# Kernel optimization log

Measured on AMD Instinct MI355X. Metric: run time of the kernel, lower is better.

## Reference

```python
import jax, jax.numpy as jnp
import numpy as np

T = 2048        # num tokens
HID = 2048      # hidden_size
HQ = 16         # num_heads
HKV = 8         # num_kv_heads
D = 128         # head_dim
P = 2           # power retention exponent
THETA = 10000.0 # rope base
SCALE = D ** -0.5


def setup_inputs() -> dict:
    key = jax.random.key(0)
    ks = jax.random.split(key, 8)
    s = 0.02
    return {
        "positions": jnp.arange(T, dtype=jnp.int64) if jax.config.jax_enable_x64 else jnp.arange(T, dtype=jnp.int32),
        "hidden_states": jax.random.normal(ks[0], (T, HID), jnp.float32),
        "Wq": jax.random.normal(ks[1], (HID, HQ * D), jnp.float32) * s,
        "bq": jnp.zeros((HQ * D,), jnp.float32),
        "Wk": jax.random.normal(ks[2], (HID, HKV * D), jnp.float32) * s,
        "bk": jnp.zeros((HKV * D,), jnp.float32),
        "Wv": jax.random.normal(ks[3], (HID, HKV * D), jnp.float32) * s,
        "bv": jnp.zeros((HKV * D,), jnp.float32),
        "Wg": jax.random.normal(ks[4], (HID, HKV), jnp.float32) * s,
        "bg": jnp.zeros((HKV,), jnp.float32),
        "Wo": jax.random.normal(ks[5], (HQ * D, HID), jnp.float32) * s,
        "bo": jnp.zeros((HID,), jnp.float32),
    }


def _rope_neox(x, pos):
    # x: [T, H, D], pos: [T]; rotate-half (neox) style, rotary_dim == head_dim
    half = D // 2
    inv_freq = 1.0 / (THETA ** (jnp.arange(0, D, 2, dtype=jnp.float32) / D))  # [D/2]
    freqs = pos.astype(jnp.float32)[:, None] * inv_freq                        # [T, D/2]
    cos = jnp.cos(freqs)[:, None, :]
    sin = jnp.sin(freqs)[:, None, :]
    x1, x2 = x[..., :half], x[..., half:]
    return jnp.concatenate([x1 * cos - x2 * sin, x2 * cos + x1 * sin], axis=-1)


def reference(positions, hidden_states, Wq, bq, Wk, bk, Wv, bv, Wg, bg, Wo, bo):
    # QKVG projections
    q = (hidden_states @ Wq + bq).reshape(T, HQ, D)
    k = (hidden_states @ Wk + bk).reshape(T, HKV, D)
    v = (hidden_states @ Wv + bv).reshape(T, HKV, D)
    g = hidden_states @ Wg + bg            # [T, HKV], one gate scalar per kv head

    # RoPE on q/k, logsigmoid gate in fp32
    q = _rope_neox(q, positions)
    k = _rope_neox(k, positions)
    g = jax.nn.log_sigmoid(g.astype(jnp.float32))   # [T, HKV], <= 0
    G = jnp.cumsum(g, axis=0)                       # [T, HKV] cumulative log-decay

    # GQA: expand kv heads to query heads
    rep = HQ // HKV
    k = jnp.repeat(k, rep, axis=1)   # [T, HQ, D]
    v = jnp.repeat(v, rep, axis=1)
    G = jnp.repeat(G, rep, axis=1)   # [T, HQ]

    # Power retention (quadratic attention form, seq_len <= switch_over_seq_len):
    # W_ij = (scale * q_i . k_j)^p * exp(G_i - G_j), causal j <= i
    S = jnp.einsum('thd,shd->hts', q, k) * SCALE      # [H, T, T]
    S = S ** P
    Gh = G.T                                          # [H, T]
    mask = jnp.tril(jnp.ones((T, T), dtype=bool))
    diff = jnp.where(mask[None], Gh[:, :, None] - Gh[:, None, :], -jnp.inf)
    W = S * jnp.exp(diff)                             # decay<=1 inside mask, 0 outside

    out = jnp.einsum('hts,shd->thd', W, v)            # [T, H, D]
    out = out.reshape(T, HQ * D) @ Wo + bo            # o_proj
    return out
```

## Files before the change

### kernel.cpp

```cpp
#include <hip/hip_runtime.h>
#include <hip/hip_bf16.h>
#include <math.h>

#define T_SEQ 2048
#define HID 2048
#define HQ 16
#define HKV 8
#define D_HEAD 128
#define HALF 64
#define SCALE_F 0.08838834764831845f
#define PROJW 4096

typedef __attribute__((ext_vector_type(8))) short bf16x8;
typedef __attribute__((ext_vector_type(4))) float f32x4;

static __device__ __forceinline__ short f2bf(float x) {
  unsigned u = __builtin_bit_cast(unsigned, x);
  unsigned r = (u + 0x7FFF + ((u >> 16) & 1)) >> 16;
  return (short)r;
}
static __device__ __forceinline__ float bf2f(unsigned short u) {
  unsigned v = ((unsigned)u) << 16;
  return __builtin_bit_cast(float, v);
}

#define GLDS(gsrc, ldst) \
  __builtin_amdgcn_global_load_lds((const __attribute__((address_space(1))) void*)(gsrc), \
                                   (__attribute__((address_space(3))) void*)(ldst), 16, 0, 0)

__global__ __launch_bounds__(256)
void cvt_bf16(const float* __restrict__ in, short* __restrict__ out, int n4)
{
  int i = blockIdx.x * blockDim.x + threadIdx.x;
  if (i >= n4) return;
  float4 v = reinterpret_cast<const float4*>(in)[i];
  short4 o;
  o.x = f2bf(v.x); o.y = f2bf(v.y); o.z = f2bf(v.z); o.w = f2bf(v.w);
  reinterpret_cast<short4*>(out)[i] = o;
}

__global__ __launch_bounds__(256)
void transpose_to_bf16(const float* __restrict__ in, short* __restrict__ out,
                       int N, int out_ld)
{
  __shared__ float tile[32][33];
  const int k0 = blockIdx.y * 32, n0 = blockIdx.x * 32;
  const int r = threadIdx.x >> 5, c = threadIdx.x & 31;
  #pragma unroll
  for (int i = 0; i < 4; ++i)
    tile[r + i * 8][c] = in[(size_t)(k0 + r + i * 8) * N + n0 + c];
  __syncthreads();
  #pragma unroll
  for (int i = 0; i < 4; ++i)
    out[(size_t)(n0 + r + i * 8) * out_ld + k0 + c] = f2bf(tile[c][r + i * 8]);
}

__global__ __launch_bounds__(256)
void pack_bias(const float* __restrict__ bq, const float* __restrict__ bk,
               const float* __restrict__ bv, float* __restrict__ bcat)
{
  const int i = blockIdx.x * 256 + threadIdx.x;
  bcat[i] = (i < 2048) ? bq[i] : ((i < 3072) ? bk[i - 2048] : bv[i - 3072]);
}

__global__ __launch_bounds__(256)
void add_f32(float* __restrict__ out, const float* __restrict__ part, int n4)
{
  int i = blockIdx.x * blockDim.x + threadIdx.x;
  if (i >= n4) return;
  float4 a = reinterpret_cast<float4*>(out)[i];
  const float4 b = reinterpret_cast<const float4*>(part)[i];
  a.x += b.x; a.y += b.y; a.z += b.z; a.w += b.w;
  reinterpret_cast<float4*>(out)[i] = a;
}

template <bool OBF>
__global__ __launch_bounds__(256)
void gemm_bf16(const short* __restrict__ A, const short* __restrict__ BT,
               const float* __restrict__ bias, void* __restrict__ Cout0,
               void* __restrict__ Cout1, int N, int Kst, int klen)
{
  __shared__ short As[2][128 * 32];
  __shared__ short Bs[2][128 * 32];
  const int tid = threadIdx.x;
  const int wave = tid >> 6, lane = tid & 63;
  const int bm0 = blockIdx.y * 128, bn0 = blockIdx.x * 128;
  const int z = blockIdx.z;
  const int koff = z * klen;
  const int wm = (wave >> 1) * 64, wn = (wave & 1) * 64;

  const int srow = wave * 32 + (lane >> 2);
  const int scol = (lane & 3) * 8;
  const short* Abase = A + (size_t)(bm0 + srow) * Kst + koff + scol;
  const short* Bbase = BT + (size_t)(bn0 + srow) * Kst + koff + scol;

  f32x4 acc[4][4] = {};

  const int nk = klen >> 5;
#define STAGE(buf, k0)                                                        \
  do {                                                                        \
    GLDS(Abase + (k0), &As[buf][(wave * 32) * 32]);                           \
    GLDS(Abase + (k0) + (size_t)16 * Kst, &As[buf][(wave * 32 + 16) * 32]);   \
    GLDS(Bbase + (k0), &Bs[buf][(wave * 32) * 32]);                           \
    GLDS(Bbase + (k0) + (size_t)16 * Kst, &Bs[buf][(wave * 32 + 16) * 32]);   \
  } while (0)

  STAGE(0, 0);
  __syncthreads();

  const int kof = (lane >> 4) * 8;
  const int rA = wm + (lane & 15);
  const int rB = wn + (lane & 15);

  for (int t = 0; t < nk; ++t) {
    const int cur = t & 1;
    if (t + 1 < nk) STAGE(cur ^ 1, (t + 1) << 5);
    bf16x8 af[4], bfr[4];
    #pragma unroll
    for (int i = 0; i < 4; ++i) {
      af[i]  = *reinterpret_cast<const bf16x8*>(&As[cur][(rA + i * 16) * 32 + kof]);
      bfr[i] = *reinterpret_cast<const bf16x8*>(&Bs[cur][(rB + i * 16) * 32 + kof]);
    }
    #pragma unroll
    for (int i = 0; i < 4; ++i)
      #pragma unroll
      for (int j = 0; j < 4; ++j)
        acc[i][j] = __builtin_amdgcn_mfma_f32_16x16x32_bf16(af[i], bfr[j], acc[i][j], 0, 0, 0);
    __syncthreads();
  }

  void* Cout = z ? Cout1 : Cout0;
  const int crow = wm + (lane >> 4) * 4;
  const int ccol = wn + (lane & 15);
  #pragma unroll
  for (int j = 0; j < 4; ++j) {
    const int col = bn0 + ccol + j * 16;
    const float b = z ? 0.f : bias[col];
    #pragma unroll
    for (int i = 0; i < 4; ++i)
      #pragma unroll
      for (int r = 0; r < 4; ++r) {
        const int row = bm0 + crow + i * 16 + r;
        const float v = acc[i][j][r] + b;
        if constexpr (OBF)
          ((short*)Cout)[(size_t)row * N + col] = f2bf(v);
        else
          ((float*)Cout)[(size_t)row * N + col] = v;
      }
  }
#undef STAGE
}

__global__ __launch_bounds__(256)
void gproj_kernel(const float* __restrict__ hs, const float* __restrict__ Wg,
                  const float* __restrict__ bg, float* __restrict__ gT)
{
  const int t = blockIdx.x, tid = threadIdx.x;
  __shared__ float red[256][9];
  float a[8] = {0.f, 0.f, 0.f, 0.f, 0.f, 0.f, 0.f, 0.f};
  for (int cc = tid; cc < HID; cc += 256) {
    const float hv = hs[(size_t)t * HID + cc];
    const float4 w0 = *reinterpret_cast<const float4*>(Wg + (size_t)cc * 8);
    const float4 w1 = *reinterpret_cast<const float4*>(Wg + (size_t)cc * 8 + 4);
    a[0] = fmaf(hv, w0.x, a[0]); a[1] = fmaf(hv, w0.y, a[1]);
    a[2] = fmaf(hv, w0.z, a[2]); a[3] = fmaf(hv, w0.w, a[3]);
    a[4] = fmaf(hv, w1.x, a[4]); a[5] = fmaf(hv, w1.y, a[5]);
    a[6] = fmaf(hv, w1.z, a[6]); a[7] = fmaf(hv, w1.w, a[7]);
  }
  #pragma unroll
  for (int j = 0; j < 8; ++j) red[tid][j] = a[j];
  __syncthreads();
  for (int s = 128; s >= 1; s >>= 1) {
    if (tid < s) {
      #pragma unroll
      for (int j = 0; j < 8; ++j) red[tid][j] += red[tid + s][j];
    }
    __syncthreads();
  }
  if (tid < 8) {
    const float x = red[0][tid] + bg[tid];
    const float nx = -x;
    const float sp = (nx > 20.f) ? nx : log1pf(expf(nx));
    gT[(size_t)tid * T_SEQ + t] = -sp;
  }
}

__global__ __launch_bounds__(512)
void gscan_kernel(const float* __restrict__ gT, float* __restrict__ Gct)
{
  const int h = blockIdx.x;
  const int tid = threadIdx.x;
  const int wid = tid >> 6, lane = tid & 63;
  __shared__ float wsum[8];

  const float4 v = reinterpret_cast<const float4*>(gT + (size_t)h * T_SEQ)[tid];
  const float p0 = v.x, p1 = p0 + v.y, p2 = p1 + v.z, p3 = p2 + v.w;

  float sc = p3;
  #pragma unroll
  for (int off = 1; off < 64; off <<= 1) {
    const float o = __shfl_up(sc, off, 64);
    if (lane >= off) sc += o;
  }
  if (lane == 63) wsum[wid] = sc;
  __syncthreads();
  float wof = 0.f;
  #pragma unroll
  for (int w = 0; w < 8; ++w) wof += (w < wid) ? wsum[w] : 0.f;

  const float excl = wof + sc - p3;
  reinterpret_cast<float4*>(Gct + (size_t)h * T_SEQ)[tid] =
      make_float4(excl + p0, excl + p1, excl + p2, excl + p3);
}

__global__ __launch_bounds__(192)
void rope_kernel(short* __restrict__ proj)
{
  const int t = blockIdx.x;
  __shared__ float cs[64], sn[64];
  if (threadIdx.x < 64) {
    const int i = threadIdx.x;
    const float f = (float)t * powf(10000.0f, -(float)i / 64.0f);
    cs[i] = cosf(f); sn[i] = sinf(f);
  }
  __syncthreads();
  const int u = threadIdx.x;
  const int hh = u >> 3, ch = u & 7;
  short* base = proj + (size_t)t * PROJW +
                ((hh < HQ) ? hh * D_HEAD : 2048 + (hh - HQ) * D_HEAD);
  bf16x8 x1 = *reinterpret_cast<bf16x8*>(base + ch * 8);
  bf16x8 x2 = *reinterpret_cast<bf16x8*>(base + HALF + ch * 8);
  #pragma unroll
  for (int j = 0; j < 8; ++j) {
    const float a = bf2f((unsigned short)x1[j]);
    const float b = bf2f((unsigned short)x2[j]);
    const float cc = cs[ch * 8 + j], ss = sn[ch * 8 + j];
    x1[j] = f2bf(a * cc - b * ss);
    x2[j] = f2bf(b * cc + a * ss);
  }
  *reinterpret_cast<bf16x8*>(base + ch * 8) = x1;
  *reinterpret_cast<bf16x8*>(base + HALF + ch * 8) = x2;
}

__global__ __launch_bounds__(256)
void vtrans_kernel(const unsigned short* __restrict__ proj, unsigned short* __restrict__ vt)
{
  __shared__ unsigned short tile[32][33];
  const int tt = blockIdx.x * 32, dd = blockIdx.y * 32, hk = blockIdx.z;
  const int c = threadIdx.x & 31, r0 = (threadIdx.x >> 5) * 4;
  #pragma unroll
  for (int i = 0; i < 4; ++i)
    tile[r0 + i][c] = proj[(size_t)(tt + r0 + i) * PROJW + 3072 + hk * 128 + dd + c];
  __syncthreads();
  #pragma unroll
  for (int i = 0; i < 4; ++i)
    vt[(size_t)(hk * 128 + dd + r0 + i) * T_SEQ + tt + c] = tile[c][r0 + i];
}

__global__ __launch_bounds__(256, 1)
void attn_mfma(const short* __restrict__ proj, const short* __restrict__ vt,
               const float* __restrict__ Gct, short* __restrict__ outb)
{
  __shared__ __align__(16) char smem[86528];
  const int hk = blockIdx.x;
  const int tb = blockIdx.y * 64;
  const int tid = threadIdx.x;
  const int wid = tid >> 6, lane = tid & 63;
  const int c = lane & 15, g = lane >> 4;
  const int h = 2 * hk + (wid >> 1);
  const int tw = tb + (wid & 1) * 32;
  const float* Gh = Gct + (size_t)hk * T_SEQ;

  const float glim = Gh[tb] + 90.0f;
  int lo = 0, hi = tb;
  while (lo < hi) {
    const int mid = (lo + hi) >> 1;
    if (Gh[mid] > glim) lo = mid + 1; else hi = mid;
  }
  const int sfirst = lo & ~63;
  const int nst = ((tb - sfirst) >> 6) + 1;

  bf16x8 qf[2][4];
  #pragma unroll
  for (int tt = 0; tt < 2; ++tt)
    #pragma unroll
    for (int kb = 0; kb < 4; ++kb)
      qf[tt][kb] = *reinterpret_cast<const bf16x8*>(
          proj + (size_t)(tw + 16 * tt + c) * PROJW + h * D_HEAD + kb * 32 + g * 8);
  const float gt0 = Gh[tw + c];
  const float gt1 = Gh[tw + 16 + c];
  const float gtw = Gh[tw];
  const int twmax = tw + 31;

  f32x4 accv[2][8] = {};

#define ASTG(buf, s64)                                                                   \
  do {                                                                                   \
    _Pragma("unroll")                                                                    \
    for (int i2 = 0; i2 < 4; ++i2) {                                                     \
      const int cid = tid + 256 * i2;                                                    \
      const int kr = cid >> 4, kc = cid & 15;                                            \
      GLDS(proj + (size_t)((s64) + kr) * PROJW + 2048 + hk * 128 + ((kc ^ (kr & 7)) * 8),\
           smem + (buf) * 16384 + cid * 16);                                             \
      const int vr = cid >> 3, vc = cid & 7;                                             \
      GLDS(vt + (size_t)(hk * 128 + vr) * T_SEQ + (s64) + ((vc ^ (vr & 7)) * 8),         \
           smem + 32768 + (buf) * 16384 + cid * 16);                                     \
    }                                                                                    \
    if (tid < 64) ((float*)(smem + 86016))[(buf) * 64 + tid] = Gh[(s64) + tid];          \
  } while (0)

  ASTG(0, sfirst);
  __syncthreads();

  for (int i = 0; i < nst; ++i) {
    const int cur = i & 1;
    if (i + 1 < nst) ASTG(cur ^ 1, sfirst + (i + 1) * 64);
    const int sbase64 = sfirst + i * 64;
    const float* Gss = (const float*)(smem + 86016) + cur * 64;
    char* Pmy = smem + 65536 + wid * 5120;

    #pragma unroll
    for (int st = 0; st < 2; ++st) {
      const int s0 = sbase64 + st * 32;
      if (s0 > twmax) continue;
      if (gtw - Gss[st * 32 + 31] < -90.0f) continue;

      bf16x8 kf[2][4];
      #pragma unroll
      for (int sg = 0; sg < 2; ++sg)
        #pragma unroll
        for (int kb = 0; kb < 4; ++kb) {
          const int row = st * 32 + 16 * sg + c;
          const int byt = (row * 256 + kb * 64 + g * 16) ^ ((c & 7) << 4);
          kf[sg][kb] = *reinterpret_cast<const bf16x8*>(smem + cur * 16384 + byt);
        }
      f32x4 sa[2][2] = {};
      #pragma unroll
      for (int kb = 0; kb < 4; ++kb)
        #pragma unroll
        for (int sg = 0; sg < 2; ++sg)
          #pragma unroll
          for (int tt = 0; tt < 2; ++tt)
            sa[sg][tt] = __builtin_amdgcn_mfma_f32_16x16x32_bf16(
                kf[sg][kb], qf[tt][kb], sa[sg][tt], 0, 0, 0);

      #pragma unroll
      for (int sg = 0; sg < 2; ++sg) {
        const float4 gs = *reinterpret_cast<const float4*>(&Gss[st * 32 + sg * 16 + g * 4]);
        const float gsv[4] = {gs.x, gs.y, gs.z, gs.w};
        #pragma unroll
        for (int tt = 0; tt < 2; ++tt) {
          const int tg = tw + 16 * tt + c;
          const float gt = tt ? gt1 : gt0;
          const int sg0 = s0 + sg * 16 + g * 4;
          float w[4];
          #pragma unroll
          for (int r = 0; r < 4; ++r) {
            const float dv = sa[sg][tt][r] * SCALE_F;
            const float ww = dv * dv * __expf(gt - gsv[r]);
            w[r] = (sg0 + r <= tg) ? ww : 0.0f;
          }
          uint2 pv;
          pv.x = ((unsigned)(unsigned short)f2bf(w[1]) << 16) | (unsigned short)f2bf(w[0]);
          pv.y = ((unsigned)(unsigned short)f2bf(w[3]) << 16) | (unsigned short)f2bf(w[2]);
          *reinterpret_cast<uint2*>(Pmy + st * 2560 + (c + 16 * tt) * 80 + 8 * g + 32 * sg) = pv;
        }
      }
      asm volatile("s_waitcnt lgkmcnt(0)" ::: "memory");
      __builtin_amdgcn_sched_barrier(0);

      bf16x8 pf[2];
      #pragma unroll
      for (int tt = 0; tt < 2; ++tt)
        pf[tt] = *reinterpret_cast<const bf16x8*>(Pmy + st * 2560 + (c + 16 * tt) * 80 + g * 16);

      #pragma unroll
      for (int db = 0; db < 8; ++db) {
        const int row = 16 * db + c;
        const int byt = (row * 128 + st * 64 + g * 16) ^ ((c & 7) << 4);
        const bf16x8 vf = *reinterpret_cast<const bf16x8*>(smem + 32768 + cur * 16384 + byt);
        #pragma unroll
        for (int tt = 0; tt < 2; ++tt)
          accv[tt][db] = __builtin_amdgcn_mfma_f32_16x16x32_bf16(pf[tt], vf, accv[tt][db], 0, 0, 0);
      }
    }
    __syncthreads();
  }

  char* Wme = smem + wid * 8704;
  #pragma unroll
  for (int tt = 0; tt < 2; ++tt)
    #pragma unroll
    for (int db = 0; db < 8; ++db)
      #pragma unroll
      for (int r = 0; r < 4; ++r)
        *reinterpret_cast<short*>(Wme + (16 * tt + 4 * g + r) * 272 + (16 * db + c) * 2)
            = f2bf(accv[tt][db][r]);
  asm volatile("s_waitcnt lgkmcnt(0)" ::: "memory");
  __builtin_amdgcn_sched_barrier(0);
  #pragma unroll
  for (int e = 0; e < 8; ++e) {
    const int idx = e * 64 + lane;
    const int tr = idx >> 4, d0 = (idx & 15) * 8;
    const bf16x8 vv = *reinterpret_cast<const bf16x8*>(Wme + tr * 272 + d0 * 2);
    *reinterpret_cast<bf16x8*>(outb + ((size_t)(tw + tr) * HQ + h) * D_HEAD + d0) = vv;
  }
#undef ASTG
}

extern "C" void kernel_launch(void* const* d_in, const int* in_sizes, int n_in,
                              void* d_out, int out_size, void* d_ws, size_t ws_size,
                              hipStream_t stream)
{
  const float* hs = (const float*)d_in[1];
  const float* Wq = (const float*)d_in[2];
  const float* bq = (const float*)d_in[3];
  const float* Wk = (const float*)d_in[4];
  const float* bk = (const float*)d_in[5];
  const float* Wv = (const float*)d_in[6];
  const float* bv = (const float*)d_in[7];
  const float* Wg = (const float*)d_in[8];
  const float* bg = (const float*)d_in[9];
  const float* Wo = (const float*)d_in[10];
  const float* bo = (const float*)d_in[11];
  float* outp = (float*)d_out;

  short* proj  = (short*)d_ws;
  short* vtb   = proj + (size_t)T_SEQ * PROJW;
  float* gT    = (float*)(vtb + (size_t)HKV * D_HEAD * T_SEQ);
  float* Gct   = gT + 16384;
  float* bcat  = Gct + 16384;
  short* hsb   = (short*)(bcat + 4096);
  short* BTall = hsb + (size_t)2048 * 2048;
  short* WoT     = BTall;
  short* attnout = hsb;
  float* partial = (float*)proj;

  cvt_bf16<<<4096, 256, 0, stream>>>(hs, hsb, 1048576);
  transpose_to_bf16<<<dim3(64, 64), 256, 0, stream>>>(Wq, BTall, 2048, 2048);
  transpose_to_bf16<<<dim3(32, 64), 256, 0, stream>>>(Wk, BTall + (size_t)2048 * 2048, 1024, 2048);
  transpose_to_bf16<<<dim3(32, 64), 256, 0, stream>>>(Wv, BTall + (size_t)3072 * 2048, 1024, 2048);
  pack_bias<<<16, 256, 0, stream>>>(bq, bk, bv, bcat);

  gemm_bf16<true><<<dim3(32, 16, 1), 256, 0, stream>>>(
      hsb, BTall, bcat, proj, proj, PROJW, 2048, 2048);

  transpose_to_bf16<<<dim3(64, 64), 256, 0, stream>>>(Wo, WoT, 2048, 2048);

  gproj_kernel<<<2048, 256, 0, stream>>>(hs, Wg, bg, gT);
  gscan_kernel<<<8, 512, 0, stream>>>(gT, Gct);

  rope_kernel<<<2048, 192, 0, stream>>>(proj);
  vtrans_kernel<<<dim3(64, 4, 8), 256, 0, stream>>>((const unsigned short*)proj,
                                                    (unsigned short*)vtb);

  attn_mfma<<<dim3(8, 32), 256, 0, stream>>>(proj, vtb, Gct, attnout);

  gemm_bf16<false><<<dim3(16, 16, 2), 256, 0, stream>>>(
      attnout, WoT, bo, outp, partial, 2048, 2048, 1024);
  add_f32<<<4096, 256, 0, stream>>>(outp, partial, 1048576);
}
```

Baseline: 149.6 us.

## Merge weight transposes, deepen GEMM pipeline, drop split-K output GEMM

```diff
diff --git a/kernel.cpp b/kernel.cpp
--- a/kernel.cpp
+++ b/kernel.cpp
@@ -40,19 +40,29 @@
 }
 
 __global__ __launch_bounds__(256)
-void transpose_to_bf16(const float* __restrict__ in, short* __restrict__ out,
-                       int N, int out_ld)
-{
+void transpose_all(const float* __restrict__ Wq, const float* __restrict__ Wk,
+                   const float* __restrict__ Wv, const float* __restrict__ Wo,
+                   short* __restrict__ BTall, short* __restrict__ WoT)
+{
+  const int bx = blockIdx.x;
+  const int k0 = blockIdx.y * 32;
+  const float* src; short* dst; int Nsrc, n0;
+  if (bx < 64)       { src = Wq; Nsrc = 2048; dst = BTall;                       n0 = bx * 32; }
+  else if (bx < 96)  { src = Wk; Nsrc = 1024; dst = BTall + (size_t)2048 * 2048; n0 = (bx - 64) * 32; }
+  else if (bx < 128) { src = Wv; Nsrc = 1024; dst = BTall + (size_t)3072 * 2048; n0 = (bx - 96) * 32; }
+  else               { src = Wo; Nsrc = 2048; dst = WoT;                         n0 = (bx - 128) * 32; }
+
   __shared__ float tile[32][33];
-  const int k0 = blockIdx.y * 32, n0 = blockIdx.x * 32;
   const int r = threadIdx.x >> 5, c = threadIdx.x & 31;
   #pragma unroll
   for (int i = 0; i < 4; ++i)
-    tile[r + i * 8][c] = in[(size_t)(k0 + r + i * 8) * N + n0 + c];
-  __syncthreads();
-  #pragma unroll
-  for (int i = 0; i < 4; ++i)
-    out[(size_t)(n0 + r + i * 8) * out_ld + k0 + c] = f2bf(tile[c][r + i * 8]);
+    tile[r + i * 8][c] = src[(size_t)(k0 + r + i * 8) * Nsrc + n0 + c];
+  __syncthreads();
+  const int n = threadIdx.x >> 3, k4 = (threadIdx.x & 7) * 4;
+  short4 o;
+  o.x = f2bf(tile[k4 + 0][n]); o.y = f2bf(tile[k4 + 1][n]);
+  o.z = f2bf(tile[k4 + 2][n]); o.w = f2bf(tile[k4 + 3][n]);
+  *reinterpret_cast<short4*>(&dst[(size_t)(n0 + n) * 2048 + k0 + k4]) = o;
 }
 
 __global__ __launch_bounds__(256)
@@ -63,58 +73,49 @@
   bcat[i] = (i < 2048) ? bq[i] : ((i < 3072) ? bk[i - 2048] : bv[i - 3072]);
 }
 
-__global__ __launch_bounds__(256)
-void add_f32(float* __restrict__ out, const float* __restrict__ part, int n4)
-{
-  int i = blockIdx.x * blockDim.x + threadIdx.x;
-  if (i >= n4) return;
-  float4 a = reinterpret_cast<float4*>(out)[i];
-  const float4 b = reinterpret_cast<const float4*>(part)[i];
-  a.x += b.x; a.y += b.y; a.z += b.z; a.w += b.w;
-  reinterpret_cast<float4*>(out)[i] = a;
-}
-
 template <bool OBF>
 __global__ __launch_bounds__(256)
 void gemm_bf16(const short* __restrict__ A, const short* __restrict__ BT,
-               const float* __restrict__ bias, void* __restrict__ Cout0,
-               void* __restrict__ Cout1, int N, int Kst, int klen)
-{
-  __shared__ short As[2][128 * 32];
-  __shared__ short Bs[2][128 * 32];
+               const float* __restrict__ bias, void* __restrict__ Cout,
+               int N, int K)
+{
+  __shared__ short As[4][128 * 32];
+  __shared__ short Bs[4][128 * 32];
   const int tid = threadIdx.x;
   const int wave = tid >> 6, lane = tid & 63;
   const int bm0 = blockIdx.y * 128, bn0 = blockIdx.x * 128;
-  const int z = blockIdx.z;
-  const int koff = z * klen;
   const int wm = (wave >> 1) * 64, wn = (wave & 1) * 64;
 
   const int srow = wave * 32 + (lane >> 2);
   const int scol = (lane & 3) * 8;
-  const short* Abase = A + (size_t)(bm0 + srow) * Kst + koff + scol;
-  const short* Bbase = BT + (size_t)(bn0 + srow) * Kst + koff + scol;
+  const short* Abase = A + (size_t)(bm0 + srow) * K + scol;
+  const short* Bbase = BT + (size_t)(bn0 + srow) * K + scol;
 
   f32x4 acc[4][4] = {};
-
-  const int nk = klen >> 5;
-#define STAGE(buf, k0)                                                        \
+  const int nk = K >> 5;
+
+#define STAGE(buf, kk)                                                        \
   do {                                                                        \
-    GLDS(Abase + (k0), &As[buf][(wave * 32) * 32]);                           \
-    GLDS(Abase + (k0) + (size_t)16 * Kst, &As[buf][(wave * 32 + 16) * 32]);   \
-    GLDS(Bbase + (k0), &Bs[buf][(wave * 32) * 32]);                           \
-    GLDS(Bbase + (k0) + (size_t)16 * Kst, &Bs[buf][(wave * 32 + 16) * 32]);   \
+    GLDS(Abase + ((kk) << 5), &As[buf][(wave * 32) * 32]);                    \
+    GLDS(Abase + ((kk) << 5) + (size_t)16 * K, &As[buf][(wave * 32 + 16) * 32]); \
+    GLDS(Bbase + ((kk) << 5), &Bs[buf][(wave * 32) * 32]);                    \
+    GLDS(Bbase + ((kk) << 5) + (size_t)16 * K, &Bs[buf][(wave * 32 + 16) * 32]); \
   } while (0)
 
   STAGE(0, 0);
-  __syncthreads();
+  STAGE(1, 1);
+  asm volatile("s_waitcnt vmcnt(4)" ::: "memory");
+  asm volatile("s_barrier" ::: "memory");
+  __builtin_amdgcn_sched_barrier(0);
 
   const int kof = (lane >> 4) * 8;
   const int rA = wm + (lane & 15);
   const int rB = wn + (lane & 15);
 
   for (int t = 0; t < nk; ++t) {
-    const int cur = t & 1;
-    if (t + 1 < nk) STAGE(cur ^ 1, (t + 1) << 5);
+    const int cur = t & 3;
+    if (t + 2 < nk) STAGE((t + 2) & 3, t + 2);
+
     bf16x8 af[4], bfr[4];
     #pragma unroll
     for (int i = 0; i < 4; ++i) {
@@ -126,16 +127,21 @@
       #pragma unroll
       for (int j = 0; j < 4; ++j)
         acc[i][j] = __builtin_amdgcn_mfma_f32_16x16x32_bf16(af[i], bfr[j], acc[i][j], 0, 0, 0);
-    __syncthreads();
-  }
-
-  void* Cout = z ? Cout1 : Cout0;
+
+    if (t + 1 < nk) {
+      if (t + 2 < nk) asm volatile("s_waitcnt vmcnt(4)" ::: "memory");
+      else            asm volatile("s_waitcnt vmcnt(0)" ::: "memory");
+      asm volatile("s_barrier" ::: "memory");
+      __builtin_amdgcn_sched_barrier(0);
+    }
+  }
+
   const int crow = wm + (lane >> 4) * 4;
   const int ccol = wn + (lane & 15);
   #pragma unroll
   for (int j = 0; j < 4; ++j) {
     const int col = bn0 + ccol + j * 16;
-    const float b = z ? 0.f : bias[col];
+    const float b = bias[col];
     #pragma unroll
     for (int i = 0; i < 4; ++i)
       #pragma unroll
@@ -432,23 +438,18 @@
   float* bcat  = Gct + 16384;
   short* hsb   = (short*)(bcat + 4096);
   short* BTall = hsb + (size_t)2048 * 2048;
-  short* WoT     = BTall;
+  short* WoT   = BTall + (size_t)4096 * 2048;
   short* attnout = hsb;
-  float* partial = (float*)proj;
 
   cvt_bf16<<<4096, 256, 0, stream>>>(hs, hsb, 1048576);
-  transpose_to_bf16<<<dim3(64, 64), 256, 0, stream>>>(Wq, BTall, 2048, 2048);
-  transpose_to_bf16<<<dim3(32, 64), 256, 0, stream>>>(Wk, BTall + (size_t)2048 * 2048, 1024, 2048);
-  transpose_to_bf16<<<dim3(32, 64), 256, 0, stream>>>(Wv, BTall + (size_t)3072 * 2048, 1024, 2048);
+  transpose_all<<<dim3(192, 64), 256, 0, stream>>>(Wq, Wk, Wv, Wo, BTall, WoT);
   pack_bias<<<16, 256, 0, stream>>>(bq, bk, bv, bcat);
-
-  gemm_bf16<true><<<dim3(32, 16, 1), 256, 0, stream>>>(
-      hsb, BTall, bcat, proj, proj, PROJW, 2048, 2048);
-
-  transpose_to_bf16<<<dim3(64, 64), 256, 0, stream>>>(Wo, WoT, 2048, 2048);
 
   gproj_kernel<<<2048, 256, 0, stream>>>(hs, Wg, bg, gT);
   gscan_kernel<<<8, 512, 0, stream>>>(gT, Gct);
+
+  gemm_bf16<true><<<dim3(32, 16), 256, 0, stream>>>(
+      hsb, BTall, bcat, proj, PROJW, 2048);
 
   rope_kernel<<<2048, 192, 0, stream>>>(proj);
   vtrans_kernel<<<dim3(64, 4, 8), 256, 0, stream>>>((const unsigned short*)proj,
@@ -456,7 +457,6 @@
 
   attn_mfma<<<dim3(8, 32), 256, 0, stream>>>(proj, vtb, Gct, attnout);
 
-  gemm_bf16<false><<<dim3(16, 16, 2), 256, 0, stream>>>(
-      attnout, WoT, bo, outp, partial, 2048, 2048, 1024);
-  add_f32<<<4096, 256, 0, stream>>>(outp, partial, 1048576);
-}
+  gemm_bf16<false><<<dim3(16, 16), 256, 0, stream>>>(
+      attnout, WoT, bo, outp, 2048, 2048);
+}
```

Measured after the change: 152.2 us. Within noise of the previous version (+1.8%).
